# Performance work log

Hardware: AMD Instinct MI355X
Metric: run time of the kernel (lower is better)

## Reference

```python
import jax, jax.numpy as jnp
import numpy as np
import math


def _favor(X, W, is_query):
    # X: [B,L,H,M], W: [M,M] (shared across batch, matching tf.repeat of a single QR matrix)
    M = X.shape[-1]
    dn = 1.0 / math.sqrt(math.sqrt(M))
    X = dn * X
    diag = (jnp.sum(X * X, axis=-1) * (0.5 * dn * dn))[..., None]  # [B,L,H,1]
    dot = jnp.einsum('dm,blhm->blhd', W, X)                         # [B,L,H,M]
    if is_query:
        mx = jnp.max(X, axis=-1, keepdims=True)
    else:
        mx = jnp.max(X, axis=(1, 3), keepdims=True)  # axes (-3,-1) = (L, M)
    return (1.0 / math.sqrt(M)) * jnp.exp(dot - diag - mx + 1e-8)


def _causal_attn(qs, ks, vs):
    # qs,ks: [B,L,H,M]; vs: [B,L,H,D]. Cumulative KV-state recurrence via lax.scan.
    B, L, H, M = ks.shape
    D = vs.shape[-1]

    def step(carry, x):
        sums, snorm = carry          # [B,H,M,D], [B,H,M]
        q, k, v = x                  # [B,H,M], [B,H,M], [B,H,D]
        snorm = snorm + k
        sums = sums + k[..., :, None] * v[..., None, :]
        num = jnp.einsum('bhmd,bhm->bhd', sums, q)
        den = jnp.sum(q * snorm, axis=-1, keepdims=True)
        return (sums, snorm), num / den

    init = (jnp.zeros((B, H, M, D), qs.dtype), jnp.zeros((B, H, M), qs.dtype))
    xs = (jnp.swapaxes(qs, 0, 1), jnp.swapaxes(ks, 0, 1), jnp.swapaxes(vs, 0, 1))
    _, out = jax.lax.scan(step, init, xs)   # out: [L,B,H,D]
    return jnp.swapaxes(out, 0, 1)          # [B,L,H,D]


def _make_favor_proj(rng, M):
    # Mirrors: W ~ N(0,1); Q,_ = qr(W); Q /= norm(Q, axis=-1) (TF broadcast divides columns); Q *= sqrt(M)
    W = rng.standard_normal((M, M)).astype(np.float32)
    Q, _ = np.linalg.qr(W)
    n = np.linalg.norm(Q, axis=1)          # row norms, shape (M,)
    Q = Q / n[None, :]                     # TF broadcasting quirk: divide column j by n[j]
    return jnp.asarray(Q * math.sqrt(M), dtype=jnp.float32)


def setup_inputs() -> dict:
    B, L, d_model, H = 2, 4096, 1024, 16
    M = d_model // H
    key = jax.random.key(0)
    k1, k2, k3 = jax.random.split(key, 3)
    rng = np.random.default_rng(0)

    def dense_w(dout):
        return jnp.asarray(rng.standard_normal((d_model, dout)).astype(np.float32) * 0.02)

    return {
        'queries': jax.random.normal(k1, (B, L, d_model), jnp.float32),
        'keys': jax.random.normal(k2, (B, L, d_model), jnp.float32),
        'values': jax.random.normal(k3, (B, L, d_model), jnp.float32),
        'Wq': dense_w(H * M), 'bq': jnp.zeros((H * M,), jnp.float32),
        'Wk': dense_w(H * M), 'bk': jnp.zeros((H * M,), jnp.float32),
        'Wv': dense_w(H * M), 'bv': jnp.zeros((H * M,), jnp.float32),
        'Wo': dense_w(d_model), 'bo': jnp.zeros((d_model,), jnp.float32),
        'Wfq': _make_favor_proj(rng, M),
        'Wfk': _make_favor_proj(rng, M),
        'H': H,
    }


def reference(queries, keys, values, Wq, bq, Wk, bk, Wv, bv, Wo, bo, Wfq, Wfk, H):
    N, L, _ = queries.shape
    S = keys.shape[1]
    q = (queries @ Wq + bq).reshape(N, L, H, -1)
    k = (keys @ Wk + bk).reshape(N, S, H, -1)
    v = (values @ Wv + bv).reshape(N, S, H, -1)
    Ql = _favor(q, Wfq, is_query=True)
    Kl = _favor(k, Wfk, is_query=False)
    V = _causal_attn(Ql, Kl, v)             # [N,L,H,D]
    return V.reshape(N, L, -1) @ Wo + bo    # [N,L,d_model]
```

## Files before the change

kernel.cpp:

```cpp
#include <hip/hip_runtime.h>
#include <math.h>

#define BATCH 2
#define SEQ   4096
#define DM    1024
#define NH    16
#define MD    64
#define NROW  (BATCH*SEQ)
#define RQ    (BATCH*SEQ*NH)
#define NCHUNK 64
#define CT     64
#define DN    0.35355339059327373f
#define HALF_DN2 0.0625f
#define INV_SQRT_M 0.125f
#define PITCH 72
#define STSZ  (65*64)
#define DIAG_SCALE (0.125f * 0.0625f)

typedef unsigned short ushort_t;
typedef short bf8_t __attribute__((ext_vector_type(8)));
typedef float f4_t  __attribute__((ext_vector_type(4)));
typedef ushort_t us8_t __attribute__((ext_vector_type(8)));

__device__ static inline ushort_t f2bf(float f) {
    union { float f; unsigned u; } v; v.f = f;
    unsigned r = v.u + 0x7FFFu + ((v.u >> 16) & 1u);
    return (ushort_t)(r >> 16);
}
__device__ static inline float bf2f(ushort_t u) {
    union { unsigned u; float f; } v; v.u = ((unsigned)u) << 16;
    return v.f;
}

__device__ static inline void async_ld16(const ushort_t* g, ushort_t* l) {
    __builtin_amdgcn_global_load_lds(
        (const __attribute__((address_space(1))) unsigned int*)g,
        (__attribute__((address_space(3))) unsigned int*)l,
        16, 0, 0);
}

__global__ __launch_bounds__(256) void cvt_f32_bf16(const float* __restrict__ X,
                                                    ushort_t* __restrict__ Y, int n8)
{
    int i = blockIdx.x * 256 + threadIdx.x;
    if (i >= n8) return;
    const float4* X4 = (const float4*)X;
    float4 a = X4[i * 2], b = X4[i * 2 + 1];
    us8_t o;
    o[0]=f2bf(a.x); o[1]=f2bf(a.y); o[2]=f2bf(a.z); o[3]=f2bf(a.w);
    o[4]=f2bf(b.x); o[5]=f2bf(b.y); o[6]=f2bf(b.z); o[7]=f2bf(b.w);
    *(us8_t*)&Y[i * 8] = o;
}

__global__ __launch_bounds__(256) void transpose_cvt(const float* __restrict__ W,
                                                     ushort_t* __restrict__ WT)
{
    __shared__ float t[32][33];
    const int k0 = blockIdx.x * 32, n0 = blockIdx.y * 32;
    const int tx = threadIdx.x & 31, ty = threadIdx.x >> 5;
    #pragma unroll
    for (int r = 0; r < 32; r += 8)
        t[ty + r][tx] = W[(size_t)(k0 + ty + r) * 1024 + n0 + tx];
    __syncthreads();
    #pragma unroll
    for (int r = 0; r < 32; r += 8)
        WT[(size_t)(n0 + ty + r) * 1024 + k0 + tx] = f2bf(t[tx][ty + r]);
}

template<int OBF>
__global__ __launch_bounds__(256) void gemm_bf16_mfma(
    const ushort_t* __restrict__ A, const ushort_t* __restrict__ BT,
    const float* __restrict__ bias, float* __restrict__ C,
    ushort_t* __restrict__ Cbf, int Ndim, int Kdim)
{
    __shared__ ushort_t As[128 * 64];
    __shared__ ushort_t Bs[128 * 64];
    const int tid = threadIdx.x;
    const int bm = blockIdx.y * 128, bn = blockIdx.x * 128;
    const int lane = tid & 63;
    const int wm = ((tid >> 6) >> 1) * 64, wn = ((tid >> 6) & 1) * 64;
    const int quad = lane >> 4, l15 = lane & 15;

    const int srow = tid >> 3, sch = tid & 7;
    const ushort_t* gA = A  + (size_t)(bm + srow) * Kdim + sch * 8;
    const ushort_t* gB = BT + (size_t)(bn + srow) * Kdim + sch * 8;
    ushort_t* lA = &As[srow * 64 + sch * 8];
    ushort_t* lB = &Bs[srow * 64 + sch * 8];

    f4_t acc[4][4] = {};

    for (int k0 = 0; k0 < Kdim; k0 += 64) {
        __syncthreads();
        #pragma unroll
        for (int c = 0; c < 4; ++c) {
            async_ld16(gA + (size_t)c * 32 * Kdim + k0, lA + c * 32 * 64);
            async_ld16(gB + (size_t)c * 32 * Kdim + k0, lB + c * 32 * 64);
        }
        __syncthreads();
        #pragma unroll
        for (int ks = 0; ks < 2; ++ks) {
            bf8_t af[4], bfr[4];
            #pragma unroll
            for (int i = 0; i < 4; ++i) {
                af[i]  = *(const bf8_t*)&As[(wm + i * 16 + l15) * 64 + ks * 32 + quad * 8];
                bfr[i] = *(const bf8_t*)&Bs[(wn + i * 16 + l15) * 64 + ks * 32 + quad * 8];
            }
            #pragma unroll
            for (int i = 0; i < 4; ++i)
                #pragma unroll
                for (int j = 0; j < 4; ++j)
                    acc[i][j] = __builtin_amdgcn_mfma_f32_16x16x32_bf16(
                        af[i], bfr[j], acc[i][j], 0, 0, 0);
        }
    }

    #pragma unroll
    for (int j = 0; j < 4; ++j) {
        const int col = bn + wn + j * 16 + l15;
        const float bb = bias[col];
        #pragma unroll
        for (int i = 0; i < 4; ++i) {
            const int row0 = bm + wm + i * 16 + quad * 4;
            #pragma unroll
            for (int r = 0; r < 4; ++r) {
                float v = acc[i][j][r] + bb;
                if (OBF) Cbf[(size_t)(row0 + r) * Ndim + col] = f2bf(v);
                else     C[(size_t)(row0 + r) * Ndim + col] = v;
            }
        }
    }
}

__global__ __launch_bounds__(256) void kmax_part_bf(const ushort_t* __restrict__ K,
                                                    float* __restrict__ partial)
{
    const int bh = blockIdx.x >> 6, slice = blockIdx.x & 63;
    const int b = bh >> 4, h = bh & 15;
    const int tid = threadIdx.x;
    const size_t base = (size_t)(b * SEQ + slice * 64) * DM + h * MD;
    float mv = -3.4e38f;
    #pragma unroll
    for (int i = 0; i < 2; ++i) {
        int idx = tid + i * 256;
        int row = idx >> 3, ch = idx & 7;
        us8_t v = *(const us8_t*)&K[base + (size_t)row * DM + ch * 8];
        #pragma unroll
        for (int j = 0; j < 8; ++j) mv = fmaxf(mv, bf2f(v[j]));
    }
    #pragma unroll
    for (int off = 32; off; off >>= 1) mv = fmaxf(mv, __shfl_xor(mv, off));
    __shared__ float red[4];
    if ((tid & 63) == 0) red[tid >> 6] = mv;
    __syncthreads();
    if (tid == 0)
        partial[blockIdx.x] = fmaxf(fmaxf(red[0], red[1]), fmaxf(red[2], red[3]));
}

__global__ __launch_bounds__(64) void kmax_final(const float* __restrict__ partial,
                                                 float* __restrict__ km)
{
    float mv = partial[blockIdx.x * 64 + threadIdx.x];
    #pragma unroll
    for (int off = 32; off; off >>= 1) mv = fmaxf(mv, __shfl_xor(mv, off));
    if (threadIdx.x == 0) km[blockIdx.x] = DN * mv;
}

__global__ __launch_bounds__(256) void favor_mfma(
    ushort_t* __restrict__ X, const float* __restrict__ Wf,
    const float* __restrict__ km, int is_query)
{
    __shared__ ushort_t Xs[64 * PITCH];
    __shared__ ushort_t Ws[64 * PITCH];
    __shared__ float ssp[64][4], mxp[64][4];
    __shared__ float diag[64], mxr[64];
    const int tid = threadIdx.x;
    const int lane = tid & 63, w = tid >> 6;
    const int quad = lane >> 4, l15 = lane & 15;
    const int rbase = blockIdx.x * 64;

    #pragma unroll
    for (int r = 0; r < 2; ++r) {
        int idx = tid + r * 256;
        int row = idx >> 3, ch = idx & 7;
        *(us8_t*)&Xs[row * PITCH + ch * 8] =
            *(const us8_t*)&X[(size_t)(rbase + row) * 64 + ch * 8];
    }
    const float4* Wf4 = (const float4*)Wf;
    #pragma unroll
    for (int i = 0; i < 4; ++i) {
        int f4i = tid + i * 256;
        int row = f4i >> 4, q4 = f4i & 15;
        float4 wv = Wf4[f4i];
        Ws[row * PITCH + q4 * 4 + 0] = f2bf(DN * wv.x);
        Ws[row * PITCH + q4 * 4 + 1] = f2bf(DN * wv.y);
        Ws[row * PITCH + q4 * 4 + 2] = f2bf(DN * wv.z);
        Ws[row * PITCH + q4 * 4 + 3] = f2bf(DN * wv.w);
    }
    __syncthreads();

    {
        const int row = tid >> 2, seg = tid & 3;
        const us8_t* xp = (const us8_t*)&Xs[row * PITCH + seg * 16];
        us8_t a = xp[0], b2 = xp[1];
        float ss = 0.f, mx = -3.4e38f;
        #pragma unroll
        for (int j = 0; j < 8; ++j) {
            float x0 = bf2f(a[j]), x1 = bf2f(b2[j]);
            ss += x0 * x0 + x1 * x1;
            mx = fmaxf(mx, fmaxf(x0, x1));
        }
        ssp[row][seg] = ss;
        mxp[row][seg] = mx;
    }
    __syncthreads();
    if (tid < 64) {
        float s = ssp[tid][0] + ssp[tid][1] + ssp[tid][2] + ssp[tid][3];
        diag[tid] = s * DIAG_SCALE;
        if (is_query) {
            float m = fmaxf(fmaxf(mxp[tid][0], mxp[tid][1]),
                            fmaxf(mxp[tid][2], mxp[tid][3]));
            mxr[tid] = DN * m;
        } else {
            int rg = rbase + tid;
            int h = rg & (NH - 1);
            int b = rg >> 16;
            mxr[tid] = km[b * NH + h];
        }
    }
    __syncthreads();

    bf8_t xf[2];
    #pragma unroll
    for (int ks = 0; ks < 2; ++ks)
        xf[ks] = *(const bf8_t*)&Xs[(w * 16 + l15) * PITCH + ks * 32 + quad * 8];
    f4_t acc[4] = {};
    #pragma unroll
    for (int dt = 0; dt < 4; ++dt)
        #pragma unroll
        for (int ks = 0; ks < 2; ++ks) {
            bf8_t wfr = *(const bf8_t*)&Ws[(dt * 16 + l15) * PITCH + ks * 32 + quad * 8];
            acc[dt] = __builtin_amdgcn_mfma_f32_16x16x32_bf16(xf[ks], wfr, acc[dt], 0, 0, 0);
        }
    __syncthreads();

    #pragma unroll
    for (int r = 0; r < 4; ++r) {
        int row = w * 16 + quad * 4 + r;
        float d_ = diag[row], m_ = mxr[row];
        #pragma unroll
        for (int dt = 0; dt < 4; ++dt) {
            float e = acc[dt][r] - d_ - m_ + 1e-8f;
            X[(size_t)(rbase + row) * 64 + dt * 16 + l15] = f2bf(INV_SQRT_M * expf(e));
        }
    }
}

__global__ __launch_bounds__(256) void chunk_sums_mfma(
    const ushort_t* __restrict__ Kbf, const ushort_t* __restrict__ Vbf,
    float* __restrict__ ST)
{
    const int bx = blockIdx.x;
    const int c = bx & 63, h = (bx >> 6) & 15, b = bx >> 10;
    __shared__ ushort_t Kt[64 * PITCH];
    __shared__ ushort_t Vt[80 * PITCH];
    const int tid = threadIdx.x;
    const int lane = tid & 63, w = tid >> 6;
    const int quad = lane >> 4, l15 = lane & 15;

    const size_t gbase = ((size_t)(b * SEQ + c * CT)) * DM + h * MD;
    #pragma unroll
    for (int r = 0; r < 2; ++r) {
        int ch = w + r * 4;
        int t = lane;
        us8_t kv = *(const us8_t*)&Kbf[gbase + (size_t)t * DM + ch * 8];
        us8_t vv = *(const us8_t*)&Vbf[gbase + (size_t)t * DM + ch * 8];
        #pragma unroll
        for (int j = 0; j < 8; ++j) {
            Kt[(ch * 8 + j) * PITCH + t] = kv[j];
            Vt[(ch * 8 + j) * PITCH + t] = vv[j];
        }
    }
    if (tid < 64) Vt[64 * PITCH + tid] = (ushort_t)0x3F80;
    __syncthreads();

    float* Sg = ST + (size_t)((b * NH + h) * NCHUNK + c) * STSZ;

    bf8_t vf[2];
    #pragma unroll
    for (int ks = 0; ks < 2; ++ks)
        vf[ks] = *(const bf8_t*)&Vt[(w * 16 + l15) * PITCH + ks * 32 + quad * 8];
    f4_t acc[4] = {};
    #pragma unroll
    for (int mt = 0; mt < 4; ++mt)
        #pragma unroll
        for (int ks = 0; ks < 2; ++ks) {
            bf8_t kf = *(const bf8_t*)&Kt[(mt * 16 + l15) * PITCH + ks * 32 + quad * 8];
            acc[mt] = __builtin_amdgcn_mfma_f32_16x16x32_bf16(vf[ks], kf, acc[mt], 0, 0, 0);
        }
    #pragma unroll
    for (int mt = 0; mt < 4; ++mt)
        #pragma unroll
        for (int r = 0; r < 4; ++r)
            Sg[(w * 16 + quad * 4 + r) * 64 + mt * 16 + l15] = acc[mt][r];

    if (w == 0) {
        bf8_t vf4[2];
        #pragma unroll
        for (int ks = 0; ks < 2; ++ks)
            vf4[ks] = *(const bf8_t*)&Vt[(64 + l15) * PITCH + ks * 32 + quad * 8];
        f4_t accz[4] = {};
        #pragma unroll
        for (int mt = 0; mt < 4; ++mt)
            #pragma unroll
            for (int ks = 0; ks < 2; ++ks) {
                bf8_t kf = *(const bf8_t*)&Kt[(mt * 16 + l15) * PITCH + ks * 32 + quad * 8];
                accz[mt] = __builtin_amdgcn_mfma_f32_16x16x32_bf16(vf4[ks], kf, accz[mt], 0, 0, 0);
            }
        if (quad == 0) {
            #pragma unroll
            for (int mt = 0; mt < 4; ++mt)
                Sg[64 * 64 + mt * 16 + l15] = accz[mt][0];
        }
    }
}

__global__ __launch_bounds__(256) void prefix_scan_st(float* __restrict__ ST)
{
    const int sb = blockIdx.x / 17;
    const int e = (blockIdx.x % 17) * 256 + threadIdx.x;
    if (e >= STSZ) return;
    float* p = ST + (size_t)sb * NCHUNK * STSZ + e;
    float run = 0.f;
    for (int c = 0; c < NCHUNK; ++c) {
        float cur = p[(size_t)c * STSZ];
        p[(size_t)c * STSZ] = run;
        run += cur;
    }
}

__global__ __launch_bounds__(256) void intra_attn_mfma(
    const ushort_t* __restrict__ Qbf, const ushort_t* __restrict__ Kbf,
    const ushort_t* __restrict__ Vbf, const float* __restrict__ ST,
    ushort_t* __restrict__ Obf)
{
    const int bx = blockIdx.x;
    const int c = bx & 63, h = (bx >> 6) & 15, b = bx >> 10;
    __shared__ ushort_t Qs[64 * PITCH];
    __shared__ ushort_t Ks[64 * PITCH];
    __shared__ ushort_t Vt[80 * PITCH];
    __shared__ ushort_t St[80 * PITCH];
    __shared__ float dens[64];
    const int tid = threadIdx.x;
    const int lane = tid & 63, w = tid >> 6;
    const int quad = lane >> 4, l15 = lane & 15;

    const size_t gbase = ((size_t)(b * SEQ + c * CT)) * DM + h * MD;

    #pragma unroll
    for (int r = 0; r < 2; ++r) {
        int idx = tid + r * 256;
        int row = idx >> 3, ch = idx & 7;
        us8_t qv = *(const us8_t*)&Qbf[gbase + (size_t)row * DM + ch * 8];
        us8_t kv = *(const us8_t*)&Kbf[gbase + (size_t)row * DM + ch * 8];
        *(us8_t*)&Qs[row * PITCH + ch * 8] = qv;
        *(us8_t*)&Ks[row * PITCH + ch * 8] = kv;
    }
    #pragma unroll
    for (int r = 0; r < 2; ++r) {
        int ch = w + r * 4;
        int t = lane;
        us8_t vv = *(const us8_t*)&Vbf[gbase + (size_t)t * DM + ch * 8];
        #pragma unroll
        for (int j = 0; j < 8; ++j) Vt[(ch * 8 + j) * PITCH + t] = vv[j];
    }
    #pragma unroll
    for (int r = 0; r < 4; ++r) {
        int idx = tid + r * 256;
        int row = 64 + (idx >> 6), t = idx & 63;
        Vt[row * PITCH + t] = (row == 64) ? (ushort_t)0x3F80 : (ushort_t)0;
    }
    const float* Sg = ST + (size_t)((b * NH + h) * NCHUNK + c) * STSZ;
    for (int r = 0; r < 17; ++r) {
        int idx = tid + r * 256;
        if (idx < STSZ) {
            int d = idx >> 6, m = idx & 63;
            St[d * PITCH + m] = f2bf(Sg[idx]);
        }
    }
    #pragma unroll
    for (int r = 0; r < 4; ++r) {
        int idx = tid + r * 256;
        if (idx < 15 * 64) {
            int row = 65 + (idx >> 6), m = idx & 63;
            St[row * PITCH + m] = 0;
        }
    }
    __syncthreads();

    bf8_t qf[2];
    #pragma unroll
    for (int ks = 0; ks < 2; ++ks)
        qf[ks] = *(const bf8_t*)&Qs[(w * 16 + l15) * PITCH + ks * 32 + quad * 8];
    f4_t accA[4] = {};
    #pragma unroll
    for (int jt = 0; jt < 4; ++jt)
        #pragma unroll
        for (int ks = 0; ks < 2; ++ks) {
            bf8_t kf = *(const bf8_t*)&Ks[(jt * 16 + l15) * PITCH + ks * 32 + quad * 8];
            accA[jt] = __builtin_amdgcn_mfma_f32_16x16x32_bf16(qf[ks], kf, accA[jt], 0, 0, 0);
        }
    __syncthreads();
    #pragma unroll
    for (int jt = 0; jt < 4; ++jt) {
        int j = jt * 16 + l15;
        #pragma unroll
        for (int r = 0; r < 4; ++r) {
            int i = w * 16 + quad * 4 + r;
            float a = (j <= i) ? accA[jt][r] : 0.f;
            Ks[i * PITCH + j] = f2bf(a);
        }
    }
    __syncthreads();

    bf8_t af[2];
    #pragma unroll
    for (int ks = 0; ks < 2; ++ks)
        af[ks] = *(const bf8_t*)&Ks[(w * 16 + l15) * PITCH + ks * 32 + quad * 8];
    f4_t acc[5] = {};
    #pragma unroll
    for (int dt = 0; dt < 5; ++dt)
        #pragma unroll
        for (int ks = 0; ks < 2; ++ks) {
            bf8_t sf = *(const bf8_t*)&St[(dt * 16 + l15) * PITCH + ks * 32 + quad * 8];
            acc[dt] = __builtin_amdgcn_mfma_f32_16x16x32_bf16(qf[ks], sf, acc[dt], 0, 0, 0);
            bf8_t vf = *(const bf8_t*)&Vt[(dt * 16 + l15) * PITCH + ks * 32 + quad * 8];
            acc[dt] = __builtin_amdgcn_mfma_f32_16x16x32_bf16(af[ks], vf, acc[dt], 0, 0, 0);
        }
    if (l15 == 0) {
        #pragma unroll
        for (int r = 0; r < 4; ++r) dens[w * 16 + quad * 4 + r] = acc[4][r];
    }
    __syncthreads();

    #pragma unroll
    for (int r = 0; r < 4; ++r) {
        int i = w * 16 + quad * 4 + r;
        float inv = 1.0f / dens[i];
        #pragma unroll
        for (int dt = 0; dt < 4; ++dt)
            Obf[gbase + (size_t)i * DM + dt * 16 + l15] = f2bf(acc[dt][r] * inv);
    }
}

extern "C" void kernel_launch(void* const* d_in, const int* in_sizes, int n_in,
                              void* d_out, int out_size, void* d_ws, size_t ws_size,
                              hipStream_t stream)
{
    const float* queries = (const float*)d_in[0];
    const float* keys    = (const float*)d_in[1];
    const float* values  = (const float*)d_in[2];
    const float* Wq = (const float*)d_in[3];  const float* bq = (const float*)d_in[4];
    const float* Wk = (const float*)d_in[5];  const float* bk = (const float*)d_in[6];
    const float* Wv = (const float*)d_in[7];  const float* bv = (const float*)d_in[8];
    const float* Wo = (const float*)d_in[9];  const float* bo = (const float*)d_in[10];

    float* ws = (float*)d_ws;
    float* STb = ws;
    float* km  = STb + (size_t)32 * NCHUNK * STSZ;
    float* kpart = km + 64;
    ushort_t* qbf = (ushort_t*)(kpart + 2048);
    ushort_t* kbf = qbf + (size_t)NROW * DM;
    ushort_t* vbf = kbf + (size_t)NROW * DM;
    ushort_t* obf = vbf + (size_t)NROW * DM;
    ushort_t* xcvt = obf + (size_t)NROW * DM;
    ushort_t* wT  = xcvt + (size_t)NROW * DM;
    ushort_t* WqT = wT;
    ushort_t* WkT = wT + (size_t)DM * DM;
    ushort_t* WvT = wT + (size_t)2 * DM * DM;
    ushort_t* WoT = wT + (size_t)3 * DM * DM;

    dim3 gtr(32, 32);
    transpose_cvt<<<gtr, 256, 0, stream>>>(Wq, WqT);
    transpose_cvt<<<gtr, 256, 0, stream>>>(Wk, WkT);
    transpose_cvt<<<gtr, 256, 0, stream>>>(Wv, WvT);
    transpose_cvt<<<gtr, 256, 0, stream>>>(Wo, WoT);

    const int n8 = NROW * DM / 8;
    dim3 gcvt(n8 / 256);
    dim3 ggemm(DM / 128, NROW / 128);

    cvt_f32_bf16<<<gcvt, 256, 0, stream>>>(queries, xcvt, n8);
    gemm_bf16_mfma<1><<<ggemm, 256, 0, stream>>>(xcvt, WqT, bq, nullptr, qbf, DM, DM);
    cvt_f32_bf16<<<gcvt, 256, 0, stream>>>(keys, xcvt, n8);
    gemm_bf16_mfma<1><<<ggemm, 256, 0, stream>>>(xcvt, WkT, bk, nullptr, kbf, DM, DM);
    cvt_f32_bf16<<<gcvt, 256, 0, stream>>>(values, xcvt, n8);
    gemm_bf16_mfma<1><<<ggemm, 256, 0, stream>>>(xcvt, WvT, bv, nullptr, vbf, DM, DM);

    kmax_part_bf<<<32 * 64, 256, 0, stream>>>(kbf, kpart);
    kmax_final<<<32, 64, 0, stream>>>(kpart, km);
    favor_mfma<<<RQ / 64, 256, 0, stream>>>(qbf, (const float*)d_in[11], nullptr, 1);
    favor_mfma<<<RQ / 64, 256, 0, stream>>>(kbf, (const float*)d_in[12], km, 0);

    chunk_sums_mfma<<<BATCH * NH * NCHUNK, 256, 0, stream>>>(kbf, vbf, STb);
    prefix_scan_st<<<32 * 17, 256, 0, stream>>>(STb);
    intra_attn_mfma<<<BATCH * NH * NCHUNK, 256, 0, stream>>>(qbf, kbf, vbf, STb, obf);

    gemm_bf16_mfma<0><<<ggemm, 256, 0, stream>>>(obf, WoT, bo, (float*)d_out, nullptr, DM, DM);
}
```

Measured before the change: 377.8 us.

## Fuse K-max into GEMM epilogue, Q favor into attention, store KV states in bf16

The key max reduction moves into the K projection GEMM epilogue using an order-preserving atomicMax, which removes the two kmax kernels. The query favor feature map is computed inside intra_attn_mfma, dropping a separate pass over Q. Weight transposes and the input conversions are batched into single launches. The chunk KV-state buffer and its prefix scan switch from fp32 to bf16, halving that traffic at the cost of accumulating precision loss across the 64-chunk prefix sum.

```diff
diff --git a/kernel.cpp b/kernel.cpp
--- a/kernel.cpp
+++ b/kernel.cpp
@@ -11,7 +11,6 @@
 #define NCHUNK 64
 #define CT     64
 #define DN    0.35355339059327373f
-#define HALF_DN2 0.0625f
 #define INV_SQRT_M 0.125f
 #define PITCH 72
 #define STSZ  (65*64)
@@ -39,39 +38,49 @@
         16, 0, 0);
 }
 
-__global__ __launch_bounds__(256) void cvt_f32_bf16(const float* __restrict__ X,
-                                                    ushort_t* __restrict__ Y, int n8)
-{
+__global__ __launch_bounds__(256) void prep_weights(
+    const float* __restrict__ W0, const float* __restrict__ W1,
+    const float* __restrict__ W2, const float* __restrict__ W3,
+    ushort_t* __restrict__ WT, unsigned* __restrict__ kmOrd)
+{
+    if (blockIdx.z == 0 && blockIdx.x == 0 && blockIdx.y == 0 && threadIdx.x < 32)
+        kmOrd[threadIdx.x] = 0u;
+    const float* W = blockIdx.z == 0 ? W0 : (blockIdx.z == 1 ? W1 : (blockIdx.z == 2 ? W2 : W3));
+    ushort_t* dst = WT + (size_t)blockIdx.z * DM * DM;
+    __shared__ float t[32][33];
+    const int k0 = blockIdx.x * 32, n0 = blockIdx.y * 32;
+    const int tx = threadIdx.x & 31, ty = threadIdx.x >> 5;
+    #pragma unroll
+    for (int r = 0; r < 32; r += 8)
+        t[ty + r][tx] = W[(size_t)(k0 + ty + r) * 1024 + n0 + tx];
+    __syncthreads();
+    #pragma unroll
+    for (int r = 0; r < 32; r += 8)
+        dst[(size_t)(n0 + ty + r) * 1024 + k0 + tx] = f2bf(t[tx][ty + r]);
+}
+
+__global__ __launch_bounds__(256) void cvt_qkv(
+    const float* __restrict__ Q, const float* __restrict__ K,
+    const float* __restrict__ V, ushort_t* __restrict__ Y)
+{
+    const int y = blockIdx.y;
+    const float* X = y == 0 ? Q : (y == 1 ? K : V);
+    ushort_t* dst = Y + (size_t)y * NROW * DM;
     int i = blockIdx.x * 256 + threadIdx.x;
-    if (i >= n8) return;
     const float4* X4 = (const float4*)X;
     float4 a = X4[i * 2], b = X4[i * 2 + 1];
     us8_t o;
     o[0]=f2bf(a.x); o[1]=f2bf(a.y); o[2]=f2bf(a.z); o[3]=f2bf(a.w);
     o[4]=f2bf(b.x); o[5]=f2bf(b.y); o[6]=f2bf(b.z); o[7]=f2bf(b.w);
-    *(us8_t*)&Y[i * 8] = o;
-}
-
-__global__ __launch_bounds__(256) void transpose_cvt(const float* __restrict__ W,
-                                                     ushort_t* __restrict__ WT)
-{
-    __shared__ float t[32][33];
-    const int k0 = blockIdx.x * 32, n0 = blockIdx.y * 32;
-    const int tx = threadIdx.x & 31, ty = threadIdx.x >> 5;
-    #pragma unroll
-    for (int r = 0; r < 32; r += 8)
-        t[ty + r][tx] = W[(size_t)(k0 + ty + r) * 1024 + n0 + tx];
-    __syncthreads();
-    #pragma unroll
-    for (int r = 0; r < 32; r += 8)
-        WT[(size_t)(n0 + ty + r) * 1024 + k0 + tx] = f2bf(t[tx][ty + r]);
-}
-
-template<int OBF>
+    *(us8_t*)&dst[i * 8] = o;
+}
+
+template<int OBF, int KM>
 __global__ __launch_bounds__(256) void gemm_bf16_mfma(
     const ushort_t* __restrict__ A, const ushort_t* __restrict__ BT,
     const float* __restrict__ bias, float* __restrict__ C,
-    ushort_t* __restrict__ Cbf, int Ndim, int Kdim)
+    ushort_t* __restrict__ Cbf, unsigned* __restrict__ kmOrd,
+    int Ndim, int Kdim)
 {
     __shared__ ushort_t As[128 * 64];
     __shared__ ushort_t Bs[128 * 64];
@@ -114,6 +123,7 @@
         }
     }
 
+    float mx = -3.4e38f;
     #pragma unroll
     for (int j = 0; j < 4; ++j) {
         const int col = bn + wn + j * 16 + l15;
@@ -124,54 +134,32 @@
             #pragma unroll
             for (int r = 0; r < 4; ++r) {
                 float v = acc[i][j][r] + bb;
+                if (KM) mx = fmaxf(mx, v);
                 if (OBF) Cbf[(size_t)(row0 + r) * Ndim + col] = f2bf(v);
                 else     C[(size_t)(row0 + r) * Ndim + col] = v;
             }
         }
     }
-}
-
-__global__ __launch_bounds__(256) void kmax_part_bf(const ushort_t* __restrict__ K,
-                                                    float* __restrict__ partial)
-{
-    const int bh = blockIdx.x >> 6, slice = blockIdx.x & 63;
-    const int b = bh >> 4, h = bh & 15;
-    const int tid = threadIdx.x;
-    const size_t base = (size_t)(b * SEQ + slice * 64) * DM + h * MD;
-    float mv = -3.4e38f;
-    #pragma unroll
-    for (int i = 0; i < 2; ++i) {
-        int idx = tid + i * 256;
-        int row = idx >> 3, ch = idx & 7;
-        us8_t v = *(const us8_t*)&K[base + (size_t)row * DM + ch * 8];
-        #pragma unroll
-        for (int j = 0; j < 8; ++j) mv = fmaxf(mv, bf2f(v[j]));
-    }
-    #pragma unroll
-    for (int off = 32; off; off >>= 1) mv = fmaxf(mv, __shfl_xor(mv, off));
-    __shared__ float red[4];
-    if ((tid & 63) == 0) red[tid >> 6] = mv;
-    __syncthreads();
-    if (tid == 0)
-        partial[blockIdx.x] = fmaxf(fmaxf(red[0], red[1]), fmaxf(red[2], red[3]));
-}
-
-__global__ __launch_bounds__(64) void kmax_final(const float* __restrict__ partial,
-                                                 float* __restrict__ km)
-{
-    float mv = partial[blockIdx.x * 64 + threadIdx.x];
-    #pragma unroll
-    for (int off = 32; off; off >>= 1) mv = fmaxf(mv, __shfl_xor(mv, off));
-    if (threadIdx.x == 0) km[blockIdx.x] = DN * mv;
-}
-
-__global__ __launch_bounds__(256) void favor_mfma(
+    if (KM) {
+        #pragma unroll
+        for (int off = 32; off; off >>= 1) mx = fmaxf(mx, __shfl_xor(mx, off));
+        if (lane == 0) {
+            const int b = bm >> 12;
+            const int h = (bn + wn) >> 6;
+            unsigned ub = __float_as_uint(mx);
+            unsigned enc = (ub & 0x80000000u) ? ~ub : (ub | 0x80000000u);
+            atomicMax(&kmOrd[b * NH + h], enc);
+        }
+    }
+}
+
+__global__ __launch_bounds__(256) void favor_k_mfma(
     ushort_t* __restrict__ X, const float* __restrict__ Wf,
-    const float* __restrict__ km, int is_query)
+    const unsigned* __restrict__ kmOrd)
 {
     __shared__ ushort_t Xs[64 * PITCH];
     __shared__ ushort_t Ws[64 * PITCH];
-    __shared__ float ssp[64][4], mxp[64][4];
+    __shared__ float ssp[64][4];
     __shared__ float diag[64], mxr[64];
     const int tid = threadIdx.x;
     const int lane = tid & 63, w = tid >> 6;
@@ -202,30 +190,23 @@
         const int row = tid >> 2, seg = tid & 3;
         const us8_t* xp = (const us8_t*)&Xs[row * PITCH + seg * 16];
         us8_t a = xp[0], b2 = xp[1];
-        float ss = 0.f, mx = -3.4e38f;
+        float ss = 0.f;
         #pragma unroll
         for (int j = 0; j < 8; ++j) {
             float x0 = bf2f(a[j]), x1 = bf2f(b2[j]);
             ss += x0 * x0 + x1 * x1;
-            mx = fmaxf(mx, fmaxf(x0, x1));
         }
         ssp[row][seg] = ss;
-        mxp[row][seg] = mx;
     }
     __syncthreads();
     if (tid < 64) {
-        float s = ssp[tid][0] + ssp[tid][1] + ssp[tid][2] + ssp[tid][3];
-        diag[tid] = s * DIAG_SCALE;
-        if (is_query) {
-            float m = fmaxf(fmaxf(mxp[tid][0], mxp[tid][1]),
-                            fmaxf(mxp[tid][2], mxp[tid][3]));
-            mxr[tid] = DN * m;
-        } else {
-            int rg = rbase + tid;
-            int h = rg & (NH - 1);
-            int b = rg >> 16;
-            mxr[tid] = km[b * NH + h];
-        }
+        diag[tid] = (ssp[tid][0] + ssp[tid][1] + ssp[tid][2] + ssp[tid][3]) * DIAG_SCALE;
+        int rg = rbase + tid;
+        int h = rg & (NH - 1);
+        int b = rg >> 16;
+        unsigned u = kmOrd[b * NH + h];
+        unsigned bits = (u & 0x80000000u) ? (u & 0x7FFFFFFFu) : ~u;
+        mxr[tid] = DN * __uint_as_float(bits);
     }
     __syncthreads();
 
@@ -257,7 +238,7 @@
 
 __global__ __launch_bounds__(256) void chunk_sums_mfma(
     const ushort_t* __restrict__ Kbf, const ushort_t* __restrict__ Vbf,
-    float* __restrict__ ST)
+    ushort_t* __restrict__ ST)
 {
     const int bx = blockIdx.x;
     const int c = bx & 63, h = (bx >> 6) & 15, b = bx >> 10;
@@ -283,7 +264,7 @@
     if (tid < 64) Vt[64 * PITCH + tid] = (ushort_t)0x3F80;
     __syncthreads();
 
-    float* Sg = ST + (size_t)((b * NH + h) * NCHUNK + c) * STSZ;
+    ushort_t* Sg = ST + (size_t)((b * NH + h) * NCHUNK + c) * STSZ;
 
     bf8_t vf[2];
     #pragma unroll
@@ -301,7 +282,7 @@
     for (int mt = 0; mt < 4; ++mt)
         #pragma unroll
         for (int r = 0; r < 4; ++r)
-            Sg[(w * 16 + quad * 4 + r) * 64 + mt * 16 + l15] = acc[mt][r];
+            Sg[(w * 16 + quad * 4 + r) * 64 + mt * 16 + l15] = f2bf(acc[mt][r]);
 
     if (w == 0) {
         bf8_t vf4[2];
@@ -319,29 +300,29 @@
         if (quad == 0) {
             #pragma unroll
             for (int mt = 0; mt < 4; ++mt)
-                Sg[64 * 64 + mt * 16 + l15] = accz[mt][0];
-        }
-    }
-}
-
-__global__ __launch_bounds__(256) void prefix_scan_st(float* __restrict__ ST)
+                Sg[64 * 64 + mt * 16 + l15] = f2bf(accz[mt][0]);
+        }
+    }
+}
+
+__global__ __launch_bounds__(256) void prefix_scan_st(ushort_t* __restrict__ ST)
 {
     const int sb = blockIdx.x / 17;
     const int e = (blockIdx.x % 17) * 256 + threadIdx.x;
     if (e >= STSZ) return;
-    float* p = ST + (size_t)sb * NCHUNK * STSZ + e;
+    ushort_t* p = ST + (size_t)sb * NCHUNK * STSZ + e;
     float run = 0.f;
     for (int c = 0; c < NCHUNK; ++c) {
-        float cur = p[(size_t)c * STSZ];
-        p[(size_t)c * STSZ] = run;
+        float cur = bf2f(p[(size_t)c * STSZ]);
+        p[(size_t)c * STSZ] = f2bf(run);
         run += cur;
     }
 }
 
 __global__ __launch_bounds__(256) void intra_attn_mfma(
-    const ushort_t* __restrict__ Qbf, const ushort_t* __restrict__ Kbf,
-    const ushort_t* __restrict__ Vbf, const float* __restrict__ ST,
-    ushort_t* __restrict__ Obf)
+    const ushort_t* __restrict__ Qraw, const ushort_t* __restrict__ Kbf,
+    const ushort_t* __restrict__ Vbf, const ushort_t* __restrict__ ST,
+    const float* __restrict__ Wfq, ushort_t* __restrict__ Obf)
 {
     const int bx = blockIdx.x;
     const int c = bx & 63, h = (bx >> 6) & 15, b = bx >> 10;
@@ -349,7 +330,10 @@
     __shared__ ushort_t Ks[64 * PITCH];
     __shared__ ushort_t Vt[80 * PITCH];
     __shared__ ushort_t St[80 * PITCH];
-    __shared__ float dens[64];
+    __shared__ ushort_t Ws[64 * PITCH];
+    __shared__ float ssp[64][4];
+    __shared__ float mxp[64][4];
+    __shared__ float diag[64], mxr[64], dens[64];
     const int tid = threadIdx.x;
     const int lane = tid & 63, w = tid >> 6;
     const int quad = lane >> 4, l15 = lane & 15;
@@ -360,7 +344,7 @@
     for (int r = 0; r < 2; ++r) {
         int idx = tid + r * 256;
         int row = idx >> 3, ch = idx & 7;
-        us8_t qv = *(const us8_t*)&Qbf[gbase + (size_t)row * DM + ch * 8];
+        us8_t qv = *(const us8_t*)&Qraw[gbase + (size_t)row * DM + ch * 8];
         us8_t kv = *(const us8_t*)&Kbf[gbase + (size_t)row * DM + ch * 8];
         *(us8_t*)&Qs[row * PITCH + ch * 8] = qv;
         *(us8_t*)&Ks[row * PITCH + ch * 8] = kv;
@@ -379,20 +363,79 @@
         int row = 64 + (idx >> 6), t = idx & 63;
         Vt[row * PITCH + t] = (row == 64) ? (ushort_t)0x3F80 : (ushort_t)0;
     }
-    const float* Sg = ST + (size_t)((b * NH + h) * NCHUNK + c) * STSZ;
-    for (int r = 0; r < 17; ++r) {
+    const us8_t* Sg8 = (const us8_t*)(ST + (size_t)((b * NH + h) * NCHUNK + c) * STSZ);
+    #pragma unroll
+    for (int r = 0; r < 3; ++r) {
         int idx = tid + r * 256;
-        if (idx < STSZ) {
-            int d = idx >> 6, m = idx & 63;
-            St[d * PITCH + m] = f2bf(Sg[idx]);
-        }
-    }
-    #pragma unroll
-    for (int r = 0; r < 4; ++r) {
-        int idx = tid + r * 256;
-        if (idx < 15 * 64) {
-            int row = 65 + (idx >> 6), m = idx & 63;
-            St[row * PITCH + m] = 0;
+        if (idx < 520) {
+            int d = idx >> 3, mo = (idx & 7) * 8;
+            *(us8_t*)&St[d * PITCH + mo] = Sg8[idx];
+        }
+        int idx2 = idx - 520;
+        if (idx2 >= 0 && idx2 < 120) {
+            int row = 65 + (idx2 >> 3), mo = (idx2 & 7) * 8;
+            us8_t z = {};
+            *(us8_t*)&St[row * PITCH + mo] = z;
+        }
+    }
+    const float4* Wf4 = (const float4*)Wfq;
+    #pragma unroll
+    for (int i = 0; i < 4; ++i) {
+        int f4i = tid + i * 256;
+        int row = f4i >> 4, q4 = f4i & 15;
+        float4 wv = Wf4[f4i];
+        Ws[row * PITCH + q4 * 4 + 0] = f2bf(DN * wv.x);
+        Ws[row * PITCH + q4 * 4 + 1] = f2bf(DN * wv.y);
+        Ws[row * PITCH + q4 * 4 + 2] = f2bf(DN * wv.z);
+        Ws[row * PITCH + q4 * 4 + 3] = f2bf(DN * wv.w);
+    }
+    __syncthreads();
+
+    {
+        const int row = tid >> 2, seg = tid & 3;
+        const us8_t* xp = (const us8_t*)&Qs[row * PITCH + seg * 16];
+        us8_t a = xp[0], b2 = xp[1];
+        float ss = 0.f, mx = -3.4e38f;
+        #pragma unroll
+        for (int j = 0; j < 8; ++j) {
+            float x0 = bf2f(a[j]), x1 = bf2f(b2[j]);
+            ss += x0 * x0 + x1 * x1;
+            mx = fmaxf(mx, fmaxf(x0, x1));
+        }
+        ssp[row][seg] = ss;
+        mxp[row][seg] = mx;
+    }
+    __syncthreads();
+    if (tid < 64) {
+        diag[tid] = (ssp[tid][0] + ssp[tid][1] + ssp[tid][2] + ssp[tid][3]) * DIAG_SCALE;
+        mxr[tid] = DN * fmaxf(fmaxf(mxp[tid][0], mxp[tid][1]),
+                              fmaxf(mxp[tid][2], mxp[tid][3]));
+    }
+    __syncthreads();
+
+    {
+        bf8_t xf[2];
+        #pragma unroll
+        for (int ks = 0; ks < 2; ++ks)
+            xf[ks] = *(const bf8_t*)&Qs[(w * 16 + l15) * PITCH + ks * 32 + quad * 8];
+        f4_t facc[4] = {};
+        #pragma unroll
+        for (int dt = 0; dt < 4; ++dt)
+            #pragma unroll
+            for (int ks = 0; ks < 2; ++ks) {
+                bf8_t wfr = *(const bf8_t*)&Ws[(dt * 16 + l15) * PITCH + ks * 32 + quad * 8];
+                facc[dt] = __builtin_amdgcn_mfma_f32_16x16x32_bf16(xf[ks], wfr, facc[dt], 0, 0, 0);
+            }
+        __syncthreads();
+        #pragma unroll
+        for (int r = 0; r < 4; ++r) {
+            int row = w * 16 + quad * 4 + r;
+            float d_ = diag[row], m_ = mxr[row];
+            #pragma unroll
+            for (int dt = 0; dt < 4; ++dt) {
+                float e = facc[dt][r] - d_ - m_ + 1e-8f;
+                Qs[row * PITCH + dt * 16 + l15] = f2bf(INV_SQRT_M * expf(e));
+            }
         }
     }
     __syncthreads();
@@ -463,47 +506,38 @@
     const float* Wk = (const float*)d_in[5];  const float* bk = (const float*)d_in[6];
     const float* Wv = (const float*)d_in[7];  const float* bv = (const float*)d_in[8];
     const float* Wo = (const float*)d_in[9];  const float* bo = (const float*)d_in[10];
-
-    float* ws = (float*)d_ws;
-    float* STb = ws;
-    float* km  = STb + (size_t)32 * NCHUNK * STSZ;
-    float* kpart = km + 64;
-    ushort_t* qbf = (ushort_t*)(kpart + 2048);
+    const float* Wfq = (const float*)d_in[11];
+    const float* Wfk = (const float*)d_in[12];
+
+    char* ws = (char*)d_ws;
+    unsigned* kmOrd = (unsigned*)ws;
+    ushort_t* STb = (ushort_t*)(ws + 256);
+    ushort_t* qbf = STb + (size_t)32 * NCHUNK * STSZ;
     ushort_t* kbf = qbf + (size_t)NROW * DM;
     ushort_t* vbf = kbf + (size_t)NROW * DM;
     ushort_t* obf = vbf + (size_t)NROW * DM;
     ushort_t* xcvt = obf + (size_t)NROW * DM;
-    ushort_t* wT  = xcvt + (size_t)NROW * DM;
+    ushort_t* wT  = xcvt + (size_t)3 * NROW * DM;
     ushort_t* WqT = wT;
     ushort_t* WkT = wT + (size_t)DM * DM;
     ushort_t* WvT = wT + (size_t)2 * DM * DM;
     ushort_t* WoT = wT + (size_t)3 * DM * DM;
 
-    dim3 gtr(32, 32);
-    transpose_cvt<<<gtr, 256, 0, stream>>>(Wq, WqT);
-    transpose_cvt<<<gtr, 256, 0, stream>>>(Wk, WkT);
-    transpose_cvt<<<gtr, 256, 0, stream>>>(Wv, WvT);
-    transpose_cvt<<<gtr, 256, 0, stream>>>(Wo, WoT);
+    prep_weights<<<dim3(32, 32, 4), 256, 0, stream>>>(Wq, Wk, Wv, Wo, wT, kmOrd);
 
     const int n8 = NROW * DM / 8;
-    dim3 gcvt(n8 / 256);
+    cvt_qkv<<<dim3(n8 / 256, 3), 256, 0, stream>>>(queries, keys, values, xcvt);
+
     dim3 ggemm(DM / 128, NROW / 128);
-
-    cvt_f32_bf16<<<gcvt, 256, 0, stream>>>(queries, xcvt, n8);
-    gemm_bf16_mfma<1><<<ggemm, 256, 0, stream>>>(xcvt, WqT, bq, nullptr, qbf, DM, DM);
-    cvt_f32_bf16<<<gcvt, 256, 0, stream>>>(keys, xcvt, n8);
-    gemm_bf16_mfma<1><<<ggemm, 256, 0, stream>>>(xcvt, WkT, bk, nullptr, kbf, DM, DM);
-    cvt_f32_bf16<<<gcvt, 256, 0, stream>>>(values, xcvt, n8);
-    gemm_bf16_mfma<1><<<ggemm, 256, 0, stream>>>(xcvt, WvT, bv, nullptr, vbf, DM, DM);
-
-    kmax_part_bf<<<32 * 64, 256, 0, stream>>>(kbf, kpart);
-    kmax_final<<<32, 64, 0, stream>>>(kpart, km);
-    favor_mfma<<<RQ / 64, 256, 0, stream>>>(qbf, (const float*)d_in[11], nullptr, 1);
-    favor_mfma<<<RQ / 64, 256, 0, stream>>>(kbf, (const float*)d_in[12], km, 0);
+    gemm_bf16_mfma<1,0><<<ggemm, 256, 0, stream>>>(xcvt, WqT, bq, nullptr, qbf, nullptr, DM, DM);
+    gemm_bf16_mfma<1,1><<<ggemm, 256, 0, stream>>>(xcvt + (size_t)NROW * DM, WkT, bk, nullptr, kbf, kmOrd, DM, DM);
+    gemm_bf16_mfma<1,0><<<ggemm, 256, 0, stream>>>(xcvt + (size_t)2 * NROW * DM, WvT, bv, nullptr, vbf, nullptr, DM, DM);
+
+    favor_k_mfma<<<RQ / 64, 256, 0, stream>>>(kbf, Wfk, kmOrd);
 
     chunk_sums_mfma<<<BATCH * NH * NCHUNK, 256, 0, stream>>>(kbf, vbf, STb);
     prefix_scan_st<<<32 * 17, 256, 0, stream>>>(STb);
-    intra_attn_mfma<<<BATCH * NH * NCHUNK, 256, 0, stream>>>(qbf, kbf, vbf, STb, obf);
-
-    gemm_bf16_mfma<0><<<ggemm, 256, 0, stream>>>(obf, WoT, bo, (float*)d_out, nullptr, DM, DM);
-}
+    intra_attn_mfma<<<BATCH * NH * NCHUNK, 256, 0, stream>>>(qbf, kbf, vbf, STb, Wfq, obf);
+
+    gemm_bf16_mfma<0,0><<<ggemm, 256, 0, stream>>>(obf, WoT, bo, (float*)d_out, nullptr, nullptr, DM, DM);
+}
```

Measured after the change: 350.2 us. -7.3%, faster.
